# Kernel optimization log

Measured on AMD Instinct MI355X. Metric: run time of the kernel, lower is better.

Reference implementation:

```python
import jax, jax.numpy as jnp
import numpy as np

B, S, D = 2, 2048, 1024
H = 16
HD = D // H

def setup_inputs() -> dict:
    key = jax.random.key(0)
    ks = jax.random.split(key, 9)
    scale = 1.0 / np.sqrt(D)
    return {
        "qi": jax.random.normal(ks[0], (B, S, D), jnp.float32),
        "ki": jax.random.normal(ks[1], (B, S, D), jnp.float32),
        "vi": jax.random.normal(ks[2], (B, S, D), jnp.float32),
        "Wq": jax.random.normal(ks[3], (D, D), jnp.float32) * scale,
        "Wq_def": jax.random.normal(ks[4], (D, D), jnp.float32) * scale,
        "Wk": jax.random.normal(ks[5], (D, D), jnp.float32) * scale,
        "Wk_def": jax.random.normal(ks[6], (D, D), jnp.float32) * scale,
        "Wv": jax.random.normal(ks[7], (D, D), jnp.float32) * scale,
        "Wo": jax.random.normal(ks[8], (D, D), jnp.float32) * scale,
    }

def _heads(x, W):
    # torch Linear: x @ W.T, then view (B,S,H,HD) and transpose -> (B,H,S,HD)
    return (x @ W.T).reshape(B, S, H, HD).transpose(0, 2, 1, 3)

def reference(qi, ki, vi, Wq, Wq_def, Wk, Wk_def, Wv, Wo):
    q = _heads(qi, Wq)
    q_def = _heads(qi, Wq_def)
    k = _heads(ki, Wk)
    k_def = _heads(ki, Wk_def)
    v = _heads(vi, Wv)
    inv_sqrt = 1.0 / jnp.sqrt(jnp.asarray(HD, qi.dtype))
    scores = jnp.einsum('bhse,bhte->bhst', q, k) * inv_sqrt
    def_scores = jnp.einsum('bhse,bhte->bhst', q_def, k_def) * inv_sqrt
    # defeasible weights: sigmoid(def_scores).sum over t -> [B,H,S], broadcast over query dim
    def_w = jax.nn.sigmoid(def_scores).sum(axis=3)  # [B,H,S]
    attn = jax.nn.softmax(scores * def_w[:, :, None, :], axis=-1)
    attended = jnp.einsum('bhst,bhtd->bshd', attn, v).reshape(B, S, D)
    return attended @ Wo.T
```

## Files before the change

kernel.cpp:

```cpp
#include <hip/hip_runtime.h>
#include <math.h>

#define BSZ 2
#define SEQ 2048
#define DIM 1024
#define NH 16
#define HDIM 64
#define MR (BSZ*SEQ)

typedef __attribute__((ext_vector_type(8))) short bf16x8;
typedef __attribute__((ext_vector_type(4))) short bf16x4;
typedef __attribute__((ext_vector_type(4))) float floatx4;
typedef _Float16 f16x8 __attribute__((ext_vector_type(8)));

static __device__ __forceinline__ unsigned short f2bf(float x) {
    unsigned u = __float_as_uint(x);
    u += 0x7fffu + ((u >> 16) & 1u);
    return (unsigned short)(u >> 16);
}
static __device__ __forceinline__ float bf2f(unsigned short h) {
    return __uint_as_float(((unsigned)h) << 16);
}
static __device__ __forceinline__ unsigned short f2h(float x) {
    union { _Float16 h; unsigned short u; } v;
    v.h = (_Float16)x;
    return v.u;
}
static __device__ __forceinline__ float fexp2(float x) {
#if __has_builtin(__builtin_amdgcn_exp2f)
    return __builtin_amdgcn_exp2f(x);
#else
    return __expf(x * 0.69314718055994531f);
#endif
}
#define MFMA16(a,b,c) __builtin_amdgcn_mfma_f32_16x16x32_bf16((a),(b),(c),0,0,0)

static __device__ __forceinline__ floatx4 mfma_f16(bf16x8 a, bf16x8 b, floatx4 c) {
    union { bf16x8 s; f16x8 h; } ua, ub;
    ua.s = a; ub.s = b;
    return __builtin_amdgcn_mfma_f32_16x16x32_f16(ua.h, ub.h, c, 0, 0, 0);
}

static __device__ __forceinline__ floatx4 pv_mfma(bf16x4 a, bf16x4 b, floatx4 c) {
#if __has_builtin(__builtin_amdgcn_mfma_f32_16x16x16bf16_1k)
    return __builtin_amdgcn_mfma_f32_16x16x16bf16_1k(a, b, c, 0, 0, 0);
#else
    bf16x8 a8 = {a[0],a[1],a[2],a[3],0,0,0,0};
    bf16x8 b8 = {b[0],b[1],b[2],b[3],0,0,0,0};
    return MFMA16(a8, b8, c);
#endif
}

static __device__ __forceinline__ void gld16(const void* g, void* l) {
    __builtin_amdgcn_global_load_lds(
        (const __attribute__((address_space(1))) void*)g,
        (__attribute__((address_space(3))) void*)l, 16, 0, 0);
}

__global__ __launch_bounds__(256)
void conv_split(const float* p0, const float* p1, const float* p2,
                const float* p3,
                unsigned short* o0, unsigned short* o1, unsigned short* o2,
                unsigned short* o3,
                int r0, int r1, int r2, int r3)
{
    const float* pin; unsigned short* pout; int rows;
    switch (blockIdx.y) {
        case 0: pin=p0; pout=o0; rows=r0; break;
        case 1: pin=p1; pout=o1; rows=r1; break;
        case 2: pin=p2; pout=o2; rows=r2; break;
        default: pin=p3; pout=o3; rows=r3; break;
    }
    size_t idx = (size_t)blockIdx.x * 256 + threadIdx.x;
    if (idx * 4 >= (size_t)rows * DIM) return;
    size_t row = (idx * 4) >> 10;
    int col = (int)((idx * 4) & 1023);
    float4 f = *(const float4*)(pin + idx * 4);
    ushort4 h, l;
    h.x = f2bf(f.x); l.x = f2bf(f.x - bf2f(h.x));
    h.y = f2bf(f.y); l.y = f2bf(f.y - bf2f(h.y));
    h.z = f2bf(f.z); l.z = f2bf(f.z - bf2f(h.z));
    h.w = f2bf(f.w); l.w = f2bf(f.w - bf2f(h.w));
    *(ushort4*)(pout + row * 2048 + col)        = h;
    *(ushort4*)(pout + row * 2048 + 1024 + col) = l;
}

__global__ __launch_bounds__(256)
void conv_f16(const float* p0, const float* p1, const float* p2, const float* p3,
              unsigned short* o0, unsigned short* o1, unsigned short* o2,
              unsigned short* o3, int r0, int r1, int r2, int r3)
{
    const float* pin; unsigned short* pout; int rows;
    switch (blockIdx.y) {
        case 0: pin=p0; pout=o0; rows=r0; break;
        case 1: pin=p1; pout=o1; rows=r1; break;
        case 2: pin=p2; pout=o2; rows=r2; break;
        default: pin=p3; pout=o3; rows=r3; break;
    }
    size_t idx = (size_t)blockIdx.x * 256 + threadIdx.x;
    if (idx * 4 >= (size_t)rows * DIM) return;
    float4 f = *(const float4*)(pin + idx * 4);
    ushort4 h;
    h.x = f2h(f.x); h.y = f2h(f.y); h.z = f2h(f.z); h.w = f2h(f.w);
    *(ushort4*)(pout + idx * 4) = h;
}

__global__ __launch_bounds__(256)
void conv_hi(const float* p0, const float* p1, const float* p2,
             unsigned short* o0, unsigned short* o1, unsigned short* o2,
             int n0, int n1, int n2)
{
    const float* pin; unsigned short* pout; int n;
    switch (blockIdx.y) {
        case 0: pin=p0; pout=o0; n=n0; break;
        case 1: pin=p1; pout=o1; n=n1; break;
        default: pin=p2; pout=o2; n=n2; break;
    }
    size_t idx = (size_t)blockIdx.x * 256 + threadIdx.x;
    if (idx * 4 >= (size_t)n) return;
    float4 f = *(const float4*)(pin + idx * 4);
    ushort4 h;
    h.x = f2bf(f.x); h.y = f2bf(f.y); h.z = f2bf(f.z); h.w = f2bf(f.w);
    *(ushort4*)(pout + idx * 4) = h;
}

template<int EPI, bool SPLIT3, int DT>
__global__ __launch_bounds__(256)
void gemm_mfma(const unsigned short* __restrict__ A0, const unsigned short* __restrict__ A1,
               const unsigned short* __restrict__ B0, const unsigned short* __restrict__ B1,
               void* C0v, void* C1v, int lda, int ldb, int nkb)
{
    const unsigned short* A = blockIdx.z ? A1 : A0;
    const unsigned short* B = blockIdx.z ? B1 : B0;
    float* Cf = (float*)(blockIdx.z ? C1v : C0v);
    unsigned short* Cb = (unsigned short*)(blockIdx.z ? C1v : C0v);

    __shared__ __align__(16) unsigned short As[128][72];
    __shared__ __align__(16) unsigned short Bs[128][72];

    const int tid = threadIdx.x;
    const int lane = tid & 63, wv = tid >> 6;
    const int c = lane & 15, quad = lane >> 4;
    const int wm = wv >> 1, wn = wv & 1;
    const int rowBase = blockIdx.y << 7;
    const int colBase = blockIdx.x << 7;

    floatx4 acc[4][4];
#pragma unroll
    for (int i = 0; i < 4; ++i)
#pragma unroll
        for (int j = 0; j < 4; ++j) acc[i][j] = (floatx4){0.f,0.f,0.f,0.f};

    bf16x8 ar[4], br[4];
    {
#pragma unroll
        for (int i = 0; i < 4; ++i) {
            int f = tid + (i << 8);
            int r = f >> 3, kbk = (f & 7) << 3;
            ar[i] = *(const bf16x8*)(A + (size_t)(rowBase + r) * lda + kbk);
            br[i] = *(const bf16x8*)(B + (size_t)(colBase + r) * ldb + kbk);
        }
    }
    for (int kb = 0; kb < nkb; ++kb) {
        __syncthreads();
#pragma unroll
        for (int i = 0; i < 4; ++i) {
            int f = tid + (i << 8);
            int r = f >> 3, kbk = (f & 7) << 3;
            *(bf16x8*)&As[r][kbk] = ar[i];
            *(bf16x8*)&Bs[r][kbk] = br[i];
        }
        __syncthreads();
        if (kb + 1 < nkb) {
            int kn = kb + 1, aoff, boff;
            if (SPLIT3) {
                int t = kn >> 4, kk = (kn & 15) << 6;
                aoff = ((t == 1) ? 1024 : 0) + kk;
                boff = ((t == 2) ? 1024 : 0) + kk;
            } else { aoff = boff = kn << 6; }
#pragma unroll
            for (int i = 0; i < 4; ++i) {
                int f = tid + (i << 8);
                int r = f >> 3, kbk = (f & 7) << 3;
                ar[i] = *(const bf16x8*)(A + (size_t)(rowBase + r) * lda + aoff + kbk);
                br[i] = *(const bf16x8*)(B + (size_t)(colBase + r) * ldb + boff + kbk);
            }
        }
#pragma unroll
        for (int ks = 0; ks < 2; ++ks) {
            bf16x8 af[4], bfr[4];
#pragma unroll
            for (int i = 0; i < 4; ++i) {
                af[i]  = *(const bf16x8*)&As[wm*64 + i*16 + c][ks*32 + quad*8];
                bfr[i] = *(const bf16x8*)&Bs[wn*64 + i*16 + c][ks*32 + quad*8];
            }
#pragma unroll
            for (int mi = 0; mi < 4; ++mi)
#pragma unroll
                for (int ni = 0; ni < 4; ++ni) {
                    if (DT == 0) acc[mi][ni] = MFMA16(af[mi], bfr[ni], acc[mi][ni]);
                    else         acc[mi][ni] = mfma_f16(af[mi], bfr[ni], acc[mi][ni]);
                }
        }
    }
    const int row0 = rowBase + wm*64 + quad*4;
    if (EPI == 0) {
        const int col0 = colBase + wn*64 + c;
#pragma unroll
        for (int mi = 0; mi < 4; ++mi)
#pragma unroll
            for (int r = 0; r < 4; ++r) {
                size_t ro = (size_t)(row0 + mi*16 + r) * 1024 + col0;
#pragma unroll
                for (int ni = 0; ni < 4; ++ni)
                    Cf[ro + ni*16] = acc[mi][ni][r];
            }
    } else if (EPI == 1) {
        const int h = (colBase >> 6) + wn;
#pragma unroll
        for (int mi = 0; mi < 4; ++mi)
#pragma unroll
            for (int r = 0; r < 4; ++r) {
                int row = row0 + mi*16 + r;
                int b = row >> 11, s = row & 2047;
                size_t base = ((size_t)((b<<4) | h) * 2048 + s) * 128;
                const int sw = (s & 7) << 3;
#pragma unroll
                for (int ni = 0; ni < 4; ++ni) {
                    int d = ni*16 + c;
                    int dsw = d ^ sw;
                    float x = acc[mi][ni][r];
                    unsigned short hb = f2bf(x);
                    Cb[base + dsw]      = hb;
                    Cb[base + 64 + dsw] = f2bf(x - bf2f(hb));
                }
            }
    } else if (EPI == 2) {
        const int h = (colBase >> 6) + wn;
#pragma unroll
        for (int mi = 0; mi < 4; ++mi) {
            int row = row0 + mi*16;
            int b = row >> 11, s = row & 2047;
#pragma unroll
            for (int ni = 0; ni < 4; ++ni) {
                int d = ni*16 + c;
                int scol = s ^ ((d & 7) << 3);
                size_t base = ((size_t)((b<<4)|h) * 64 + d) * 2048 + scol;
                ushort4 o4;
                o4.x = f2bf(acc[mi][ni][0]); o4.y = f2bf(acc[mi][ni][1]);
                o4.z = f2bf(acc[mi][ni][2]); o4.w = f2bf(acc[mi][ni][3]);
                *(ushort4*)(Cb + base) = o4;
            }
        }
    } else {
        const int h = (colBase >> 6) + wn;
#pragma unroll
        for (int mi = 0; mi < 4; ++mi)
#pragma unroll
            for (int r = 0; r < 4; ++r) {
                int row = row0 + mi*16 + r;
                int b = row >> 11, s = row & 2047;
                size_t base = ((size_t)((b<<4) | h) * 2048 + s) * 64;
#pragma unroll
                for (int ni = 0; ni < 4; ++ni)
                    Cb[base + ni*16 + c] = f2h(acc[mi][ni][r]);
            }
    }
}

__global__ __launch_bounds__(256)
void defw_mfma(const unsigned short* __restrict__ qd,
               const unsigned short* __restrict__ kd,
               float* __restrict__ defw)
{
    __shared__ __align__(16) unsigned short Ks[64][72];
    const int tid = threadIdx.x;
    const int wv = tid >> 6, lane = tid & 63;
    const int c = lane & 15, quad = lane >> 4;
    const int bh = blockIdx.y;
    const int qbase = blockIdx.x << 7;
    const int trow = tid >> 2, seg = tid & 3;

    bf16x8 qf[2][2];
#pragma unroll
    for (int mi = 0; mi < 2; ++mi) {
        const unsigned short* qrow =
            qd + ((size_t)bh*2048 + qbase + wv*32 + mi*16 + c)*64 + quad*8;
        qf[mi][0] = *(const bf16x8*)(qrow);
        qf[mi][1] = *(const bf16x8*)(qrow + 32);
    }
    float rs[2][4] = {{0.f,0.f,0.f,0.f},{0.f,0.f,0.f,0.f}};
    const unsigned short* kbase = kd + (size_t)bh*2048*64;
    bf16x8 kpre[2];
    {
        const unsigned short* kp = kbase + (size_t)trow*64 + seg*16;
        kpre[0] = *(const bf16x8*)(kp);
        kpre[1] = *(const bf16x8*)(kp + 8);
    }
    for (int kt = 0; kt < SEQ; kt += 64) {
        __syncthreads();
        *(bf16x8*)&Ks[trow][seg*16 + 0] = kpre[0];
        *(bf16x8*)&Ks[trow][seg*16 + 8] = kpre[1];
        __syncthreads();
        if (kt + 64 < SEQ) {
            const unsigned short* kp = kbase + (size_t)(kt + 64 + trow)*64 + seg*16;
            kpre[0] = *(const bf16x8*)(kp);
            kpre[1] = *(const bf16x8*)(kp + 8);
        }
#pragma unroll
        for (int nk = 0; nk < 4; ++nk) {
            const unsigned short* kr = &Ks[16*nk + c][quad*8];
            bf16x8 k0 = *(const bf16x8*)(kr);
            bf16x8 k1 = *(const bf16x8*)(kr + 32);
#pragma unroll
            for (int mi = 0; mi < 2; ++mi) {
                floatx4 s = {0.f,0.f,0.f,0.f};
                s = mfma_f16(qf[mi][0], k0, s);
                s = mfma_f16(qf[mi][1], k1, s);
#pragma unroll
                for (int r = 0; r < 4; ++r)
                    rs[mi][r] += 1.f / (1.f + __expf(-0.125f * s[r]));
            }
        }
    }
#pragma unroll
    for (int mi = 0; mi < 2; ++mi)
#pragma unroll
        for (int r = 0; r < 4; ++r) {
            float vv = rs[mi][r];
            vv += __shfl_xor(vv, 1, 16);
            vv += __shfl_xor(vv, 2, 16);
            vv += __shfl_xor(vv, 4, 16);
            vv += __shfl_xor(vv, 8, 16);
            if (c == 0)
                defw[(size_t)bh*SEQ + qbase + wv*32 + mi*16 + 4*quad + r]
                    = vv * 0.18033688011112042f;
        }
}

__global__ __launch_bounds__(256)
void flash_mfma(const unsigned short* __restrict__ q,
                const unsigned short* __restrict__ kk,
                const unsigned short* __restrict__ vt,
                const float* __restrict__ dwg,
                unsigned short* __restrict__ o)
{
    __shared__ __align__(16) unsigned short Ks[2][64][128];
    __shared__ __align__(16) unsigned short Vs[2][64][64];
    __shared__ __align__(16) float dwL[SEQ];
    const int tid = threadIdx.x;
    const int wv = tid >> 6, lane = tid & 63;
    const int c = lane & 15, quad = lane >> 4;
    const int cswz = c & 7;
    const int bh = blockIdx.y, b = bh >> 4, h = bh & 15;
    const int qbase = blockIdx.x << 7;

    const unsigned short* kbase = kk + (size_t)bh*2048*128;
    const unsigned short* vbase = vt + (size_t)bh*64*2048;

    bf16x8 qhi[2][2], qlo[2][2];
#pragma unroll
    for (int mi = 0; mi < 2; ++mi) {
        const unsigned short* qrow =
            q + ((size_t)bh*2048 + qbase + wv*32 + mi*16 + c)*128;
        qhi[mi][0] = *(const bf16x8*)(qrow + (((quad     ) ^ cswz) << 3));
        qhi[mi][1] = *(const bf16x8*)(qrow + (((quad +  4) ^ cswz) << 3));
        qlo[mi][0] = *(const bf16x8*)(qrow + (((quad +  8) ^ cswz) << 3));
        qlo[mi][1] = *(const bf16x8*)(qrow + (((quad + 12) ^ cswz) << 3));
    }
#pragma unroll
    for (int i = 0; i < 2; ++i) {
        int flat = tid + (i << 8);
        gld16(dwg + (size_t)bh*SEQ + (size_t)flat*4,
              &dwL[(wv*64 + (i << 8)) * 4]);
    }
#pragma unroll
    for (int i = 0; i < 4; ++i) {
        int flat = tid + (i << 8);
        int r = flat >> 4, ch = flat & 15;
        gld16(kbase + (size_t)r*128 + (ch << 3),
              &Ks[0][0][0] + ((wv*64 + (i << 8)) << 3));
    }
#pragma unroll
    for (int i = 0; i < 2; ++i) {
        int flat = tid + (i << 8);
        int d = flat >> 3, ch = flat & 7;
        gld16(vbase + (size_t)d*2048 + (ch << 3),
              &Vs[0][0][0] + ((wv*64 + (i << 8)) << 3));
    }

    floatx4 Oa[4][2];
#pragma unroll
    for (int nd = 0; nd < 4; ++nd)
#pragma unroll
        for (int mi = 0; mi < 2; ++mi) Oa[nd][mi] = (floatx4){0.f,0.f,0.f,0.f};
    float mrun[2] = {-3.0e38f, -3.0e38f}, lrun[2] = {0.f, 0.f};

    for (int kt = 0; kt < SEQ; kt += 64) {
        const int cur = (kt >> 6) & 1;
        __builtin_amdgcn_s_barrier();
        if (kt + 64 < SEQ) {
            const int nb = cur ^ 1;
#pragma unroll
            for (int i = 0; i < 4; ++i) {
                int flat = tid + (i << 8);
                int r = flat >> 4, ch = flat & 15;
                gld16(kbase + (size_t)(kt + 64 + r)*128 + (ch << 3),
                      &Ks[nb][0][0] + ((wv*64 + (i << 8)) << 3));
            }
#pragma unroll
            for (int i = 0; i < 2; ++i) {
                int flat = tid + (i << 8);
                int d = flat >> 3, ch = flat & 7;
                gld16(vbase + (size_t)d*2048 + (kt + 64) + (ch << 3),
                      &Vs[nb][0][0] + ((wv*64 + (i << 8)) << 3));
            }
            asm volatile("s_waitcnt vmcnt(6)" ::: "memory");
        } else {
            asm volatile("s_waitcnt vmcnt(0)" ::: "memory");
        }
        __builtin_amdgcn_s_barrier();
        __builtin_amdgcn_sched_barrier(0);

        float z[2][4][4];
#pragma unroll
        for (int nk = 0; nk < 4; ++nk) {
            const unsigned short* krow = &Ks[cur][16*nk + c][0];
            bf16x8 kh0 = *(const bf16x8*)(krow + (((quad     ) ^ cswz) << 3));
            bf16x8 kh1 = *(const bf16x8*)(krow + (((quad +  4) ^ cswz) << 3));
            bf16x8 kl0 = *(const bf16x8*)(krow + (((quad +  8) ^ cswz) << 3));
            bf16x8 kl1 = *(const bf16x8*)(krow + (((quad + 12) ^ cswz) << 3));
            float4 d4 = *(const float4*)&dwL[kt + nk*16 + quad*4];
#pragma unroll
            for (int mi = 0; mi < 2; ++mi) {
                floatx4 s = {0.f,0.f,0.f,0.f};
                s = MFMA16(kh0, qhi[mi][0], s);
                s = MFMA16(kh1, qhi[mi][1], s);
                s = MFMA16(kh0, qlo[mi][0], s);
                s = MFMA16(kh1, qlo[mi][1], s);
                s = MFMA16(kl0, qhi[mi][0], s);
                s = MFMA16(kl1, qhi[mi][1], s);
                z[mi][nk][0] = s[0] * d4.x;
                z[mi][nk][1] = s[1] * d4.y;
                z[mi][nk][2] = s[2] * d4.z;
                z[mi][nk][3] = s[3] * d4.w;
            }
        }
#pragma unroll
        for (int mi = 0; mi < 2; ++mi) {
            float tm = z[mi][0][0];
#pragma unroll
            for (int nk = 0; nk < 4; ++nk)
#pragma unroll
                for (int r = 0; r < 4; ++r) tm = fmaxf(tm, z[mi][nk][r]);
            tm = fmaxf(tm, __shfl_xor(tm, 16));
            tm = fmaxf(tm, __shfl_xor(tm, 32));
            if (__any(tm > mrun[mi])) {
                float mn = fmaxf(mrun[mi], tm);
                float al = fexp2(mrun[mi] - mn);
                mrun[mi] = mn;
                lrun[mi] *= al;
#pragma unroll
                for (int nd = 0; nd < 4; ++nd)
#pragma unroll
                    for (int r = 0; r < 4; ++r)
                        Oa[nd][mi][r] *= al;
            }
            float rsum = 0.f;
#pragma unroll
            for (int nk = 0; nk < 4; ++nk)
#pragma unroll
                for (int r = 0; r < 4; ++r) {
                    z[mi][nk][r] = fexp2(z[mi][nk][r] - mrun[mi]);
                    rsum += z[mi][nk][r];
                }
            rsum += __shfl_xor(rsum, 16);
            rsum += __shfl_xor(rsum, 32);
            lrun[mi] += rsum;
        }
        bf16x4 pb[2][4];
#pragma unroll
        for (int mi = 0; mi < 2; ++mi)
#pragma unroll
            for (int nk = 0; nk < 4; ++nk) {
                bf16x4 p;
                p[0] = (short)f2bf(z[mi][nk][0]);
                p[1] = (short)f2bf(z[mi][nk][1]);
                p[2] = (short)f2bf(z[mi][nk][2]);
                p[3] = (short)f2bf(z[mi][nk][3]);
                pb[mi][nk] = p;
            }
#pragma unroll
        for (int ks = 0; ks < 4; ++ks) {
            const int vch = ((2*ks + (quad >> 1)) ^ cswz);
#pragma unroll
            for (int nd = 0; nd < 4; ++nd) {
                const bf16x4 va = *(const bf16x4*)
                    (&Vs[cur][nd*16 + c][0] + (vch << 3) + ((quad & 1) << 2));
#pragma unroll
                for (int mi = 0; mi < 2; ++mi)
                    Oa[nd][mi] = pv_mfma(va, pb[mi][ks], Oa[nd][mi]);
            }
        }
    }
#pragma unroll
    for (int mi = 0; mi < 2; ++mi) {
        float invl = 1.f / lrun[mi];
        int s_abs = qbase + wv*32 + mi*16 + c;
        unsigned short* orow = o + ((size_t)(b*SEQ + s_abs))*DIM + h*HDIM;
#pragma unroll
        for (int nd = 0; nd < 4; ++nd) {
            ushort4 o4;
            o4.x = f2bf(Oa[nd][mi][0] * invl);
            o4.y = f2bf(Oa[nd][mi][1] * invl);
            o4.z = f2bf(Oa[nd][mi][2] * invl);
            o4.w = f2bf(Oa[nd][mi][3] * invl);
            *(ushort4*)(orow + nd*16 + quad*4) = o4;
        }
    }
}

extern "C" void kernel_launch(void* const* d_in, const int* in_sizes, int n_in,
                              void* d_out, int out_size, void* d_ws, size_t ws_size,
                              hipStream_t stream)
{
    (void)in_sizes; (void)n_in; (void)out_size; (void)ws_size;
    const float* qi     = (const float*)d_in[0];
    const float* ki     = (const float*)d_in[1];
    const float* vi     = (const float*)d_in[2];
    const float* Wq     = (const float*)d_in[3];
    const float* Wq_def = (const float*)d_in[4];
    const float* Wk     = (const float*)d_in[5];
    const float* Wk_def = (const float*)d_in[6];
    const float* Wv     = (const float*)d_in[7];
    const float* Wo     = (const float*)d_in[8];
    float* out = (float*)d_out;

    char* ws = (char*)d_ws;
    const size_t MB = 1024 * 1024;
    unsigned short* Aqf  = (unsigned short*)(ws +  0*MB);
    unsigned short* Akf  = (unsigned short*)(ws +  8*MB);
    unsigned short* Bqdf = (unsigned short*)(ws + 16*MB);
    unsigned short* Bkdf = (unsigned short*)(ws + 18*MB);
    unsigned short* qdf  = (unsigned short*)(ws + 20*MB);
    unsigned short* kdf  = (unsigned short*)(ws + 28*MB);
    unsigned short* Aq  = (unsigned short*)(ws +  0*MB);
    unsigned short* Ak  = (unsigned short*)(ws + 16*MB);
    unsigned short* Bq  = (unsigned short*)(ws + 32*MB);
    unsigned short* Bk  = (unsigned short*)(ws + 36*MB);
    unsigned short* qs  = (unsigned short*)(ws + 40*MB);
    unsigned short* ks  = (unsigned short*)(ws + 56*MB);
    float*          dw  = (float*)(ws + 72*MB);
    unsigned short* Av  = (unsigned short*)(ws +  0*MB);
    unsigned short* Bv  = (unsigned short*)(ws +  8*MB);
    unsigned short* Bo  = (unsigned short*)(ws + 10*MB);
    unsigned short* Vt  = (unsigned short*)(ws + 12*MB);
    unsigned short* att = (unsigned short*)(ws + 20*MB);

    dim3 cb(256);
    dim3 gP(DIM/128, MR/128, 2);
    dim3 gS(DIM/128, MR/128, 1);
    dim3 gA(SEQ/128, BSZ*NH);

    conv_f16<<<dim3(4096, 4), cb, 0, stream>>>(
        qi, ki, Wq_def, Wk_def, Aqf, Akf, Bqdf, Bkdf, MR, MR, DIM, DIM);
    gemm_mfma<3, false, 1><<<gP, cb, 0, stream>>>(Aqf, Akf, Bqdf, Bkdf, qdf, kdf, 1024, 1024, 16);
    defw_mfma<<<gA, cb, 0, stream>>>(qdf, kdf, dw);
    conv_split<<<dim3(4096, 4), cb, 0, stream>>>(
        qi, ki, Wq, Wk, Aq, Ak, Bq, Bk, MR, MR, DIM, DIM);
    gemm_mfma<1, true, 0><<<gP, cb, 0, stream>>>(Aq, Ak, Bq, Bk, qs, ks, 2048, 2048, 48);
    conv_hi<<<dim3(4096, 3), cb, 0, stream>>>(vi, Wv, Wo, Av, Bv, Bo,
                                              MR*DIM, DIM*DIM, DIM*DIM);
    gemm_mfma<2, false, 0><<<gS, cb, 0, stream>>>(Av, Av, Bv, Bv, Vt, Vt, 1024, 1024, 16);
    flash_mfma<<<gA, cb, 0, stream>>>(qs, ks, Vt, dw, att);
    gemm_mfma<0, false, 0><<<gS, cb, 0, stream>>>(att, att, Bo, Bo, out, out, 1024, 1024, 16);
}
```

Measured before the change: 433.0 us.

## Use 512-thread flash blocks with one 16-row query tile per wave

The flash attention kernel now launches 512 threads (8 waves) per block, and each wave handles 16 query rows instead of 32. This halves the per-wave register state (Q fragments, O accumulators, softmax stats) and spreads the cooperative K/V/defw tile loads over more threads, aiming for more waves in flight to hide latency. It also replaces the manual bf16 rounding of P with packed v_cvt_pk_bf16_f32 instructions. The trade-off is that each K/V tile read from LDS is reused across fewer query rows per wave, and the larger block adds barrier cost.

Measured after the change: 423.9 us. 2.1% less time.

```diff
diff --git a/kernel.cpp b/kernel.cpp
--- a/kernel.cpp
+++ b/kernel.cpp
@@ -32,6 +32,12 @@
 #else
     return __expf(x * 0.69314718055994531f);
 #endif
+}
+static __device__ __forceinline__ bf16x4 pack_bf16x4(float a, float b, float c, float d) {
+    union { unsigned u[2]; bf16x4 v; } r;
+    asm("v_cvt_pk_bf16_f32 %0, %1, %2" : "=v"(r.u[0]) : "v"(a), "v"(b));
+    asm("v_cvt_pk_bf16_f32 %0, %1, %2" : "=v"(r.u[1]) : "v"(c), "v"(d));
+    return r.v;
 }
 #define MFMA16(a,b,c) __builtin_amdgcn_mfma_f32_16x16x32_bf16((a),(b),(c),0,0,0)
 
@@ -338,7 +344,7 @@
         }
 }
 
-__global__ __launch_bounds__(256)
+__global__ __launch_bounds__(512)
 void flash_mfma(const unsigned short* __restrict__ q,
                 const unsigned short* __restrict__ kk,
                 const unsigned short* __restrict__ vt,
@@ -358,43 +364,33 @@
     const unsigned short* kbase = kk + (size_t)bh*2048*128;
     const unsigned short* vbase = vt + (size_t)bh*64*2048;
 
-    bf16x8 qhi[2][2], qlo[2][2];
-#pragma unroll
-    for (int mi = 0; mi < 2; ++mi) {
+    bf16x8 qhi[2], qlo[2];
+    {
         const unsigned short* qrow =
-            q + ((size_t)bh*2048 + qbase + wv*32 + mi*16 + c)*128;
-        qhi[mi][0] = *(const bf16x8*)(qrow + (((quad     ) ^ cswz) << 3));
-        qhi[mi][1] = *(const bf16x8*)(qrow + (((quad +  4) ^ cswz) << 3));
-        qlo[mi][0] = *(const bf16x8*)(qrow + (((quad +  8) ^ cswz) << 3));
-        qlo[mi][1] = *(const bf16x8*)(qrow + (((quad + 12) ^ cswz) << 3));
-    }
+            q + ((size_t)bh*2048 + qbase + wv*16 + c)*128;
+        qhi[0] = *(const bf16x8*)(qrow + (((quad     ) ^ cswz) << 3));
+        qhi[1] = *(const bf16x8*)(qrow + (((quad +  4) ^ cswz) << 3));
+        qlo[0] = *(const bf16x8*)(qrow + (((quad +  8) ^ cswz) << 3));
+        qlo[1] = *(const bf16x8*)(qrow + (((quad + 12) ^ cswz) << 3));
+    }
+    gld16(dwg + (size_t)bh*SEQ + (size_t)tid*4, &dwL[(wv*64) * 4]);
 #pragma unroll
     for (int i = 0; i < 2; ++i) {
-        int flat = tid + (i << 8);
-        gld16(dwg + (size_t)bh*SEQ + (size_t)flat*4,
-              &dwL[(wv*64 + (i << 8)) * 4]);
-    }
-#pragma unroll
-    for (int i = 0; i < 4; ++i) {
-        int flat = tid + (i << 8);
+        int flat = tid + (i << 9);
         int r = flat >> 4, ch = flat & 15;
         gld16(kbase + (size_t)r*128 + (ch << 3),
-              &Ks[0][0][0] + ((wv*64 + (i << 8)) << 3));
-    }
-#pragma unroll
-    for (int i = 0; i < 2; ++i) {
-        int flat = tid + (i << 8);
-        int d = flat >> 3, ch = flat & 7;
+              &Ks[0][0][0] + ((wv*64 + (i << 9)) << 3));
+    }
+    {
+        int d = tid >> 3, ch = tid & 7;
         gld16(vbase + (size_t)d*2048 + (ch << 3),
-              &Vs[0][0][0] + ((wv*64 + (i << 8)) << 3));
-    }
-
-    floatx4 Oa[4][2];
-#pragma unroll
-    for (int nd = 0; nd < 4; ++nd)
-#pragma unroll
-        for (int mi = 0; mi < 2; ++mi) Oa[nd][mi] = (floatx4){0.f,0.f,0.f,0.f};
-    float mrun[2] = {-3.0e38f, -3.0e38f}, lrun[2] = {0.f, 0.f};
+              &Vs[0][0][0] + (wv*64 << 3));
+    }
+
+    floatx4 Oa[4];
+#pragma unroll
+    for (int nd = 0; nd < 4; ++nd) Oa[nd] = (floatx4){0.f,0.f,0.f,0.f};
+    float mrun = -3.0e38f, lrun = 0.f;
 
     for (int kt = 0; kt < SEQ; kt += 64) {
         const int cur = (kt >> 6) & 1;
@@ -402,27 +398,25 @@
         if (kt + 64 < SEQ) {
             const int nb = cur ^ 1;
 #pragma unroll
-            for (int i = 0; i < 4; ++i) {
-                int flat = tid + (i << 8);
+            for (int i = 0; i < 2; ++i) {
+                int flat = tid + (i << 9);
                 int r = flat >> 4, ch = flat & 15;
                 gld16(kbase + (size_t)(kt + 64 + r)*128 + (ch << 3),
-                      &Ks[nb][0][0] + ((wv*64 + (i << 8)) << 3));
-            }
-#pragma unroll
-            for (int i = 0; i < 2; ++i) {
-                int flat = tid + (i << 8);
-                int d = flat >> 3, ch = flat & 7;
+                      &Ks[nb][0][0] + ((wv*64 + (i << 9)) << 3));
+            }
+            {
+                int d = tid >> 3, ch = tid & 7;
                 gld16(vbase + (size_t)d*2048 + (kt + 64) + (ch << 3),
-                      &Vs[nb][0][0] + ((wv*64 + (i << 8)) << 3));
-            }
-            asm volatile("s_waitcnt vmcnt(6)" ::: "memory");
+                      &Vs[nb][0][0] + (wv*64 << 3));
+            }
+            asm volatile("s_waitcnt vmcnt(3)" ::: "memory");
         } else {
             asm volatile("s_waitcnt vmcnt(0)" ::: "memory");
         }
         __builtin_amdgcn_s_barrier();
         __builtin_amdgcn_sched_barrier(0);
 
-        float z[2][4][4];
+        float z[4][4];
 #pragma unroll
         for (int nk = 0; nk < 4; ++nk) {
             const unsigned short* krow = &Ks[cur][16*nk + c][0];
@@ -431,65 +425,53 @@
             bf16x8 kl0 = *(const bf16x8*)(krow + (((quad +  8) ^ cswz) << 3));
             bf16x8 kl1 = *(const bf16x8*)(krow + (((quad + 12) ^ cswz) << 3));
             float4 d4 = *(const float4*)&dwL[kt + nk*16 + quad*4];
-#pragma unroll
-            for (int mi = 0; mi < 2; ++mi) {
-                floatx4 s = {0.f,0.f,0.f,0.f};
-                s = MFMA16(kh0, qhi[mi][0], s);
-                s = MFMA16(kh1, qhi[mi][1], s);
-                s = MFMA16(kh0, qlo[mi][0], s);
-                s = MFMA16(kh1, qlo[mi][1], s);
-                s = MFMA16(kl0, qhi[mi][0], s);
-                s = MFMA16(kl1, qhi[mi][1], s);
-                z[mi][nk][0] = s[0] * d4.x;
-                z[mi][nk][1] = s[1] * d4.y;
-                z[mi][nk][2] = s[2] * d4.z;
-                z[mi][nk][3] = s[3] * d4.w;
-            }
-        }
-#pragma unroll
-        for (int mi = 0; mi < 2; ++mi) {
-            float tm = z[mi][0][0];
+            floatx4 s = {0.f,0.f,0.f,0.f};
+            s = MFMA16(kh0, qhi[0], s);
+            s = MFMA16(kh1, qhi[1], s);
+            s = MFMA16(kh0, qlo[0], s);
+            s = MFMA16(kh1, qlo[1], s);
+            s = MFMA16(kl0, qhi[0], s);
+            s = MFMA16(kl1, qhi[1], s);
+            z[nk][0] = s[0] * d4.x;
+            z[nk][1] = s[1] * d4.y;
+            z[nk][2] = s[2] * d4.z;
+            z[nk][3] = s[3] * d4.w;
+        }
+        {
+            float tm = z[0][0];
 #pragma unroll
             for (int nk = 0; nk < 4; ++nk)
 #pragma unroll
-                for (int r = 0; r < 4; ++r) tm = fmaxf(tm, z[mi][nk][r]);
+                for (int r = 0; r < 4; ++r) tm = fmaxf(tm, z[nk][r]);
             tm = fmaxf(tm, __shfl_xor(tm, 16));
             tm = fmaxf(tm, __shfl_xor(tm, 32));
-            if (__any(tm > mrun[mi])) {
-                float mn = fmaxf(mrun[mi], tm);
-                float al = fexp2(mrun[mi] - mn);
-                mrun[mi] = mn;
-                lrun[mi] *= al;
+            if (__any(tm > mrun)) {
+                float mn = fmaxf(mrun, tm);
+                float al = fexp2(mrun - mn);
+                mrun = mn;
+                lrun *= al;
 #pragma unroll
                 for (int nd = 0; nd < 4; ++nd)
 #pragma unroll
                     for (int r = 0; r < 4; ++r)
-                        Oa[nd][mi][r] *= al;
+                        Oa[nd][r] *= al;
             }
             float rsum = 0.f;
 #pragma unroll
             for (int nk = 0; nk < 4; ++nk)
 #pragma unroll
                 for (int r = 0; r < 4; ++r) {
-                    z[mi][nk][r] = fexp2(z[mi][nk][r] - mrun[mi]);
-                    rsum += z[mi][nk][r];
+                    z[nk][r] = fexp2(z[nk][r] - mrun);
+                    rsum += z[nk][r];
                 }
             rsum += __shfl_xor(rsum, 16);
             rsum += __shfl_xor(rsum, 32);
-            lrun[mi] += rsum;
-        }
-        bf16x4 pb[2][4];
-#pragma unroll
-        for (int mi = 0; mi < 2; ++mi)
-#pragma unroll
-            for (int nk = 0; nk < 4; ++nk) {
-                bf16x4 p;
-                p[0] = (short)f2bf(z[mi][nk][0]);
-                p[1] = (short)f2bf(z[mi][nk][1]);
-                p[2] = (short)f2bf(z[mi][nk][2]);
-                p[3] = (short)f2bf(z[mi][nk][3]);
-                pb[mi][nk] = p;
-            }
+            lrun += rsum;
+        }
+        bf16x4 pb[4];
+#pragma unroll
+        for (int nk = 0; nk < 4; ++nk)
+            pb[nk] = pack_bf16x4(z[nk][0], z[nk][1], z[nk][2], z[nk][3]);
 #pragma unroll
         for (int ks = 0; ks < 4; ++ks) {
             const int vch = ((2*ks + (quad >> 1)) ^ cswz);
@@ -497,24 +479,21 @@
             for (int nd = 0; nd < 4; ++nd) {
                 const bf16x4 va = *(const bf16x4*)
                     (&Vs[cur][nd*16 + c][0] + (vch << 3) + ((quad & 1) << 2));
-#pragma unroll
-                for (int mi = 0; mi < 2; ++mi)
-                    Oa[nd][mi] = pv_mfma(va, pb[mi][ks], Oa[nd][mi]);
-            }
-        }
-    }
-#pragma unroll
-    for (int mi = 0; mi < 2; ++mi) {
-        float invl = 1.f / lrun[mi];
-        int s_abs = qbase + wv*32 + mi*16 + c;
+                Oa[nd] = pv_mfma(va, pb[ks], Oa[nd]);
+            }
+        }
+    }
+    {
+        float invl = 1.f / lrun;
+        int s_abs = qbase + wv*16 + c;
         unsigned short* orow = o + ((size_t)(b*SEQ + s_abs))*DIM + h*HDIM;
 #pragma unroll
         for (int nd = 0; nd < 4; ++nd) {
             ushort4 o4;
-            o4.x = f2bf(Oa[nd][mi][0] * invl);
-            o4.y = f2bf(Oa[nd][mi][1] * invl);
-            o4.z = f2bf(Oa[nd][mi][2] * invl);
-            o4.w = f2bf(Oa[nd][mi][3] * invl);
+            o4.x = f2bf(Oa[nd][0] * invl);
+            o4.y = f2bf(Oa[nd][1] * invl);
+            o4.z = f2bf(Oa[nd][2] * invl);
+            o4.w = f2bf(Oa[nd][3] * invl);
             *(ushort4*)(orow + nd*16 + quad*4) = o4;
         }
     }
@@ -572,6 +551,6 @@
     conv_hi<<<dim3(4096, 3), cb, 0, stream>>>(vi, Wv, Wo, Av, Bv, Bo,
                                               MR*DIM, DIM*DIM, DIM*DIM);
     gemm_mfma<2, false, 0><<<gS, cb, 0, stream>>>(Av, Av, Bv, Bv, Vt, Vt, 1024, 1024, 16);
-    flash_mfma<<<gA, cb, 0, stream>>>(qs, ks, Vt, dw, att);
+    flash_mfma<<<gA, dim3(512), 0, stream>>>(qs, ks, Vt, dw, att);
     gemm_mfma<0, false, 0><<<gS, cb, 0, stream>>>(att, att, Bo, Bo, out, out, 1024, 1024, 16);
 }
```
